# Kernel optimization log

Measured on AMD Instinct MI355X. Metric: run time of the kernel, lower is better.

## Reference

```python
import jax, jax.numpy as jnp
import numpy as np

B, S = 8, 512          # batch, seq_len
D, F = 1024, 2048      # d_model, head hidden dim
H = 16                 # num_tasks (= num heads)
V = 3000               # selfies vocab
O = 1                  # head output size
INIT = 0.02


def setup_inputs() -> dict:
    key = jax.random.key(0)
    ks = jax.random.split(key, 12)
    return {
        "selfies": jax.random.randint(ks[0], (B, S), 0, V),
        "tasks": jax.random.randint(ks[1], (B, S), 0, H + 1),  # 0 -> invalid (-1)
        "values": jax.random.normal(ks[2], (B, S), jnp.float32),
        "property_mask": jax.random.randint(ks[3], (B, S), 0, 2).astype(bool),
        # shared_base params (embed + FFN -> [B,S,D])
        "emb_selfies": jax.random.normal(ks[4], (V, D), jnp.float32) * INIT,
        "emb_tasks": jax.random.normal(ks[5], (H + 1, D), jnp.float32) * INIT,
        "val_vec": jax.random.normal(ks[6], (D,), jnp.float32) * INIT,
        "Ws": jax.random.normal(ks[7], (D, D), jnp.float32) * INIT,
        "bs": jnp.zeros((D,), jnp.float32),
        # stacked per-head MLP params: Linear(D,F) -> GELU -> Linear(F,O)
        "W1": jax.random.normal(ks[8], (H, D, F), jnp.float32) * INIT,
        "b1": jnp.zeros((H, F), jnp.float32),
        "W2": jax.random.normal(ks[9], (H, F, O), jnp.float32) * INIT,
        "b2": jnp.zeros((H, O), jnp.float32),
    }


def reference(selfies, tasks, values, property_mask,
              emb_selfies, emb_tasks, val_vec, Ws, bs, W1, b1, W2, b2):
    # ---- shared_base: embed + masked token features + FFN -> [B,S,D] ----
    h = (emb_selfies[selfies] + emb_tasks[tasks] + values[..., None] * val_vec)
    h = h * property_mask[..., None].astype(h.dtype)
    shared = jax.nn.gelu(h @ Ws + bs)                      # [B,S,D]

    # ---- routing: task token -> head index, 0 means invalid (-1) ----
    head_idx = jnp.where(tasks > 0, (tasks - 1) % H, -1)   # [B,S]

    # ---- each active head runs its MLP over the FULL shared_output ----
    hid = jax.nn.gelu(jnp.einsum('bsd,hdf->bshf', shared, W1) + b1)  # [B,S,H,F]
    heads_out = jnp.einsum('bshf,hfo->bsho', hid, W2) + b2           # [B,S,H,O]

    # ---- scatter/select per token by head index; invalid -> zeros ----
    idx = jnp.clip(head_idx, 0)
    out = jnp.take_along_axis(heads_out, idx[..., None, None], axis=2)[:, :, 0, :]
    return jnp.where(head_idx[..., None] >= 0, out, jnp.zeros_like(out))
```

## Files before the change

kernel.cpp:

```cpp
#include <hip/hip_runtime.h>
#include <hip/hip_bf16.h>

#define TOK 4096
#define DD  1024
#define FF  2048
#define NH  16

typedef short bf16x8 __attribute__((ext_vector_type(8)));
typedef float f32x4  __attribute__((ext_vector_type(4)));

__device__ __forceinline__ float gelu_f(float x) {
  float u = 0.7978845608028654f * (x + 0.044715f * x * x * x);
  float e = __expf(2.0f * u);
  return 0.5f * x * (2.0f - 2.0f / (e + 1.0f));
}

__device__ __forceinline__ unsigned short f2bf(float f) {
  union { float f; unsigned u; } v; v.f = f;
  unsigned r = v.u + 0x7FFF + ((v.u >> 16) & 1);
  return (unsigned short)(r >> 16);
}
__device__ __forceinline__ unsigned pack2(float a, float b) {
  return (unsigned)f2bf(a) | ((unsigned)f2bf(b) << 16);
}

__device__ __forceinline__ void load_lds16(const void* g, void* l) {
  __builtin_amdgcn_global_load_lds(
      (const __attribute__((address_space(1))) void*)g,
      (__attribute__((address_space(3))) void*)l, 16, 0, 0);
}

__global__ __launch_bounds__(256) void route_kernel(
    const int* __restrict__ tasks, const float* __restrict__ b2,
    int* __restrict__ counts, int* __restrict__ lists, float* __restrict__ out) {
  int t = blockIdx.x * 256 + threadIdx.x;
  if (t >= TOK) return;
  int task = tasks[t];
  if (task > 0) {
    int h = (task - 1) & (NH - 1);
    int pos = atomicAdd(&counts[h], 1);
    lists[h * TOK + pos] = t;
    out[t] = b2[h];
  } else {
    out[t] = 0.0f;
  }
}

__global__ __launch_bounds__(256) void prep_x(
    const int* __restrict__ selfies, const int* __restrict__ tasks,
    const float* __restrict__ values, const int* __restrict__ pmask,
    const float* __restrict__ emb_s, const float* __restrict__ emb_t,
    const float* __restrict__ val_vec, unsigned short* __restrict__ Xb) {
  int gid = blockIdx.x * 256 + threadIdx.x;
  int kc = (gid & 127) * 8;
  int t  = gid >> 7;
  int sid = selfies[t], tsk = tasks[t];
  float v = values[t];
  float msk = pmask[t] ? 1.0f : 0.0f;
  const float* ps = emb_s + (size_t)sid * DD + kc;
  const float* pt = emb_t + (size_t)tsk * DD + kc;
  const float* pv = val_vec + kc;
  float r[8];
#pragma unroll
  for (int j = 0; j < 8; j += 4) {
    float4 a = *(const float4*)(ps + j);
    float4 b = *(const float4*)(pt + j);
    float4 c = *(const float4*)(pv + j);
    r[j + 0] = (a.x + b.x + v * c.x) * msk;
    r[j + 1] = (a.y + b.y + v * c.y) * msk;
    r[j + 2] = (a.z + b.z + v * c.z) * msk;
    r[j + 3] = (a.w + b.w + v * c.w) * msk;
  }
  uint4 o;
  o.x = pack2(r[0], r[1]); o.y = pack2(r[2], r[3]);
  o.z = pack2(r[4], r[5]); o.w = pack2(r[6], r[7]);
  *(uint4*)(Xb + (size_t)gid * 8) = o;
}

__global__ __launch_bounds__(256) void prep_w(
    const float* __restrict__ Ws, const float* __restrict__ W1,
    unsigned short* __restrict__ Wsp, unsigned short* __restrict__ W1p) {
  int cid = blockIdx.x * 256 + threadIdx.x;
  const float* src;
  unsigned short* dst;
  int stride;
  if (cid < 16 * 128 * 32 * 64) {
    int lane = cid & 63, kc2 = (cid >> 6) & 31, nt = (cid >> 11) & 127, h = cid >> 18;
    src = W1 + ((size_t)h * DD + kc2 * 32 + (lane >> 4) * 8) * FF + nt * 16 + (lane & 15);
    dst = W1p + (size_t)cid * 8;
    stride = FF;
  } else {
    int cid2 = cid - 16 * 128 * 32 * 64;
    int lane = cid2 & 63, kc2 = (cid2 >> 6) & 31, nt = cid2 >> 11;
    src = Ws + ((size_t)kc2 * 32 + (lane >> 4) * 8) * DD + nt * 16 + (lane & 15);
    dst = Wsp + (size_t)cid2 * 8;
    stride = DD;
  }
  float r[8];
#pragma unroll
  for (int j = 0; j < 8; ++j) r[j] = src[(size_t)j * stride];
  uint4 o;
  o.x = pack2(r[0], r[1]); o.y = pack2(r[2], r[3]);
  o.z = pack2(r[4], r[5]); o.w = pack2(r[6], r[7]);
  *(uint4*)dst = o;
}

__global__ __launch_bounds__(256) void gemm1_mfma(
    const unsigned short* __restrict__ Xb, const unsigned short* __restrict__ Wsp,
    const float* __restrict__ bs, unsigned short* __restrict__ shared_bf) {
  __shared__ __align__(16) unsigned short As[2 * 4 * 64 * 8];
  __shared__ __align__(16) unsigned short Bs[2 * 8 * 64 * 8];

  const int tid = threadIdx.x;
  const int lane = tid & 63, w = tid >> 6;
  const int m0 = blockIdx.x * 64;
  const int n0 = blockIdx.y * 128;
  const int q = lane >> 4, c = lane & 15;

  const unsigned short* aSrc = Xb + (size_t)(m0 + w * 16 + c) * DD + q * 8;
  unsigned short* aDst0 = As + (size_t)(0 * 256 + w * 64 + lane) * 8;
  unsigned short* aDst1 = As + (size_t)(1 * 256 + w * 64 + lane) * 8;

  const unsigned short* bBase = Wsp + ((size_t)(blockIdx.y * 8 + w * 2)) * 32 * 512 + lane * 8;
  f32x4 acc[4][2] = {};

  for (int k0 = 0; k0 < DD; k0 += 64) {
    load_lds16(aSrc + k0, aDst0);
    load_lds16(aSrc + k0 + 32, aDst1);
    const unsigned short* bk = bBase + k0 * 16;
#pragma unroll
    for (int i = 0; i < 4; ++i) {
      int kk = i >> 1, t = i & 1;
      load_lds16(bk + (size_t)t * 16384 + kk * 512,
                 Bs + (size_t)(kk * 8 + w * 2 + t) * 512 + lane * 8);
    }
    __syncthreads();
#pragma unroll
    for (int kk = 0; kk < 2; ++kk) {
      bf16x8 a[4], b[2];
#pragma unroll
      for (int mt = 0; mt < 4; ++mt)
        a[mt] = *(const bf16x8*)(As + (size_t)((kk * 4 + mt) * 64 + lane) * 8);
#pragma unroll
      for (int t = 0; t < 2; ++t)
        b[t] = *(const bf16x8*)(Bs + (size_t)((kk * 8 + w * 2 + t) * 64 + lane) * 8);
#pragma unroll
      for (int mt = 0; mt < 4; ++mt)
#pragma unroll
        for (int t = 0; t < 2; ++t)
          acc[mt][t] = __builtin_amdgcn_mfma_f32_16x16x32_bf16(a[mt], b[t], acc[mt][t], 0, 0, 0);
    }
    __syncthreads();
  }

  float bsv[2];
#pragma unroll
  for (int t = 0; t < 2; ++t) bsv[t] = bs[n0 + w * 32 + t * 16 + c];
#pragma unroll
  for (int mt = 0; mt < 4; ++mt)
#pragma unroll
    for (int t = 0; t < 2; ++t)
#pragma unroll
      for (int r = 0; r < 4; ++r) {
        int row = m0 + mt * 16 + q * 4 + r;
        int col = n0 + w * 32 + t * 16 + c;
        shared_bf[(size_t)row * DD + col] = f2bf(gelu_f(acc[mt][t][r] + bsv[t]));
      }
}

__global__ __launch_bounds__(256) void gemm2_mfma(
    const unsigned short* __restrict__ shared_bf, const unsigned short* __restrict__ W1p,
    const float* __restrict__ b1, const float* __restrict__ W2,
    const int* __restrict__ counts, const int* __restrict__ lists,
    float* __restrict__ out) {
  const int h = blockIdx.z;
  const int nt_h = counts[h];
  const int m0 = blockIdx.x * 64;
  if (m0 >= nt_h) return;
  const int fc = blockIdx.y;

  __shared__ __align__(16) unsigned short As[2 * 4 * 64 * 8];
  __shared__ __align__(16) unsigned short Bs[2 * 16 * 64 * 8];
  __shared__ int   stok[64];
  __shared__ float red[4][68];

  const int tid = threadIdx.x;
  const int lane = tid & 63, w = tid >> 6;
  const int q = lane >> 4, c = lane & 15;

  if (tid < 64) {
    int i = m0 + tid;
    stok[tid] = (i < nt_h) ? lists[h * TOK + i] : -1;
  }
  __syncthreads();

  int tokr = stok[w * 16 + c];
  if (tokr < 0) tokr = 0;
  const unsigned short* aSrc = shared_bf + (size_t)tokr * DD + q * 8;
  unsigned short* aDst0 = As + (size_t)(0 * 256 + w * 64 + lane) * 8;
  unsigned short* aDst1 = As + (size_t)(1 * 256 + w * 64 + lane) * 8;

  const unsigned short* bBase =
      W1p + ((size_t)h * 128 + fc * 16 + w * 4) * 32 * 512 + lane * 8;

  f32x4 acc[4][4] = {};

  for (int k0 = 0; k0 < DD; k0 += 64) {
    load_lds16(aSrc + k0, aDst0);
    load_lds16(aSrc + k0 + 32, aDst1);
    const unsigned short* bk = bBase + k0 * 16;
#pragma unroll
    for (int i = 0; i < 8; ++i) {
      int kk = i >> 2, t = i & 3;
      load_lds16(bk + (size_t)t * 16384 + kk * 512,
                 Bs + (size_t)(kk * 16 + w * 4 + t) * 512 + lane * 8);
    }
    __syncthreads();
#pragma unroll
    for (int kk = 0; kk < 2; ++kk) {
      bf16x8 a[4], b[4];
#pragma unroll
      for (int mt = 0; mt < 4; ++mt)
        a[mt] = *(const bf16x8*)(As + (size_t)((kk * 4 + mt) * 64 + lane) * 8);
#pragma unroll
      for (int t = 0; t < 4; ++t)
        b[t] = *(const bf16x8*)(Bs + (size_t)((kk * 16 + w * 4 + t) * 64 + lane) * 8);
#pragma unroll
      for (int mt = 0; mt < 4; ++mt)
#pragma unroll
        for (int t = 0; t < 4; ++t)
          acc[mt][t] = __builtin_amdgcn_mfma_f32_16x16x32_bf16(a[mt], b[t], acc[mt][t], 0, 0, 0);
    }
    __syncthreads();
  }

  const float* b1h = b1 + (size_t)h * FF + fc * 256 + w * 64;
  const float* w2h = W2 + (size_t)h * FF + fc * 256 + w * 64;
  float b1v[4], w2v[4];
#pragma unroll
  for (int t = 0; t < 4; ++t) { b1v[t] = b1h[t * 16 + c]; w2v[t] = w2h[t * 16 + c]; }

#pragma unroll
  for (int mt = 0; mt < 4; ++mt)
#pragma unroll
    for (int r = 0; r < 4; ++r) {
      float s = 0.0f;
#pragma unroll
      for (int t = 0; t < 4; ++t)
        s += gelu_f(acc[mt][t][r] + b1v[t]) * w2v[t];
      s += __shfl_xor(s, 1);
      s += __shfl_xor(s, 2);
      s += __shfl_xor(s, 4);
      s += __shfl_xor(s, 8);
      if (c == 0) red[w][mt * 16 + q * 4 + r] = s;
    }
  __syncthreads();

  if (tid < 64) {
    int t = stok[tid];
    if (t >= 0) {
      float s = red[0][tid] + red[1][tid] + red[2][tid] + red[3][tid];
      atomicAdd(&out[t], s);
    }
  }
}

extern "C" void kernel_launch(void* const* d_in, const int* in_sizes, int n_in,
                              void* d_out, int out_size, void* d_ws, size_t ws_size,
                              hipStream_t stream) {
  const int*   selfies = (const int*)d_in[0];
  const int*   tasks   = (const int*)d_in[1];
  const float* values  = (const float*)d_in[2];
  const int*   pmask   = (const int*)d_in[3];
  const float* emb_s   = (const float*)d_in[4];
  const float* emb_t   = (const float*)d_in[5];
  const float* val_vec = (const float*)d_in[6];
  const float* Ws      = (const float*)d_in[7];
  const float* bs      = (const float*)d_in[8];
  const float* W1      = (const float*)d_in[9];
  const float* b1      = (const float*)d_in[10];
  const float* W2      = (const float*)d_in[11];
  const float* b2      = (const float*)d_in[12];
  float* out = (float*)d_out;

  char* ws = (char*)d_ws;
  unsigned short* Xb        = (unsigned short*)ws;
  unsigned short* shared_bf = (unsigned short*)(ws + (8u << 20));
  unsigned short* Wsp       = (unsigned short*)(ws + (16u << 20));
  unsigned short* W1p       = (unsigned short*)(ws + (18u << 20));
  int* counts = (int*)(ws + (82u << 20));
  int* lists  = (int*)(ws + (82u << 20) + 256);

  hipMemsetAsync(counts, 0, NH * sizeof(int), stream);
  route_kernel<<<TOK / 256, 256, 0, stream>>>(tasks, b2, counts, lists, out);
  prep_x<<<TOK * 128 / 256, 256, 0, stream>>>(selfies, tasks, values, pmask,
                                              emb_s, emb_t, val_vec, Xb);
  prep_w<<<(16 * 128 * 32 * 64 + 64 * 32 * 64) / 256, 256, 0, stream>>>(Ws, W1, Wsp, W1p);
  gemm1_mfma<<<dim3(TOK / 64, DD / 128), 256, 0, stream>>>(Xb, Wsp, bs, shared_bf);
  gemm2_mfma<<<dim3(8, FF / 256, NH), 256, 0, stream>>>(shared_bf, W1p, b1, W2,
                                                        counts, lists, out);
}
```

Before: 354.1 us.

## Stream B fragments via registers, double-buffer A in LDS, fuse routing into prep

Both GEMM kernels now load the pre-swizzled weight fragments straight from global memory into registers with one-stage prefetch, and keep only the activation tile in a double-buffered LDS array. This cuts LDS traffic and allows one barrier per k-step instead of two. The routing kernel is folded into the embedding prep kernel to save a launch. prep_w now has each thread convert two adjacent 16-column tiles, and launch bounds ask for 2 blocks per CU. The risks are higher register pressure from the bc/bn fragment arrays and uncoalesced-latency stalls on the direct global B loads.

```diff
diff --git a/kernel.cpp b/kernel.cpp
--- a/kernel.cpp
+++ b/kernel.cpp
@@ -30,31 +30,27 @@
       (__attribute__((address_space(3))) void*)l, 16, 0, 0);
 }
 
-__global__ __launch_bounds__(256) void route_kernel(
-    const int* __restrict__ tasks, const float* __restrict__ b2,
-    int* __restrict__ counts, int* __restrict__ lists, float* __restrict__ out) {
-  int t = blockIdx.x * 256 + threadIdx.x;
-  if (t >= TOK) return;
-  int task = tasks[t];
-  if (task > 0) {
-    int h = (task - 1) & (NH - 1);
-    int pos = atomicAdd(&counts[h], 1);
-    lists[h * TOK + pos] = t;
-    out[t] = b2[h];
-  } else {
-    out[t] = 0.0f;
-  }
-}
-
-__global__ __launch_bounds__(256) void prep_x(
+__global__ __launch_bounds__(256) void prep_xr(
     const int* __restrict__ selfies, const int* __restrict__ tasks,
     const float* __restrict__ values, const int* __restrict__ pmask,
     const float* __restrict__ emb_s, const float* __restrict__ emb_t,
-    const float* __restrict__ val_vec, unsigned short* __restrict__ Xb) {
+    const float* __restrict__ val_vec, const float* __restrict__ b2,
+    unsigned short* __restrict__ Xb, int* __restrict__ counts,
+    int* __restrict__ lists, float* __restrict__ out) {
   int gid = blockIdx.x * 256 + threadIdx.x;
   int kc = (gid & 127) * 8;
   int t  = gid >> 7;
   int sid = selfies[t], tsk = tasks[t];
+  if ((gid & 127) == 0) {
+    if (tsk > 0) {
+      int h = (tsk - 1) & (NH - 1);
+      int pos = atomicAdd(&counts[h], 1);
+      lists[h * TOK + pos] = t;
+      out[t] = b2[h];
+    } else {
+      out[t] = 0.0f;
+    }
+  }
   float v = values[t];
   float msk = pmask[t] ? 1.0f : 0.0f;
   const float* ps = emb_s + (size_t)sid * DD + kc;
@@ -80,36 +76,48 @@
 __global__ __launch_bounds__(256) void prep_w(
     const float* __restrict__ Ws, const float* __restrict__ W1,
     unsigned short* __restrict__ Wsp, unsigned short* __restrict__ W1p) {
-  int cid = blockIdx.x * 256 + threadIdx.x;
-  const float* src;
-  unsigned short* dst;
+  const int W1_PAIRS = 16 * 64 * 32 * 64;
+  int cid2 = blockIdx.x * 256 + threadIdx.x;
+  const float* src0;
+  unsigned short *dst0, *dst1;
   int stride;
-  if (cid < 16 * 128 * 32 * 64) {
-    int lane = cid & 63, kc2 = (cid >> 6) & 31, nt = (cid >> 11) & 127, h = cid >> 18;
-    src = W1 + ((size_t)h * DD + kc2 * 32 + (lane >> 4) * 8) * FF + nt * 16 + (lane & 15);
-    dst = W1p + (size_t)cid * 8;
+  if (cid2 < W1_PAIRS) {
+    int lane = cid2 & 63, kc2 = (cid2 >> 6) & 31, ntp = (cid2 >> 11) & 63, h = cid2 >> 17;
+    int q = lane >> 4, c = lane & 15;
+    src0 = W1 + ((size_t)h * DD + kc2 * 32 + q * 8) * FF + ntp * 32 + c;
+    size_t c0 = (((size_t)h * 128 + ntp * 2) * 32 + kc2) * 64 + lane;
+    dst0 = W1p + c0 * 8;
+    dst1 = W1p + (c0 + 32 * 64) * 8;
     stride = FF;
   } else {
-    int cid2 = cid - 16 * 128 * 32 * 64;
-    int lane = cid2 & 63, kc2 = (cid2 >> 6) & 31, nt = cid2 >> 11;
-    src = Ws + ((size_t)kc2 * 32 + (lane >> 4) * 8) * DD + nt * 16 + (lane & 15);
-    dst = Wsp + (size_t)cid2 * 8;
+    int cid3 = cid2 - W1_PAIRS;
+    int lane = cid3 & 63, kc2 = (cid3 >> 6) & 31, ntp = cid3 >> 11;
+    int q = lane >> 4, c = lane & 15;
+    src0 = Ws + ((size_t)kc2 * 32 + q * 8) * DD + ntp * 32 + c;
+    size_t c0 = ((size_t)(ntp * 2) * 32 + kc2) * 64 + lane;
+    dst0 = Wsp + c0 * 8;
+    dst1 = Wsp + (c0 + 32 * 64) * 8;
     stride = DD;
   }
-  float r[8];
-#pragma unroll
-  for (int j = 0; j < 8; ++j) r[j] = src[(size_t)j * stride];
-  uint4 o;
-  o.x = pack2(r[0], r[1]); o.y = pack2(r[2], r[3]);
-  o.z = pack2(r[4], r[5]); o.w = pack2(r[6], r[7]);
-  *(uint4*)dst = o;
-}
-
-__global__ __launch_bounds__(256) void gemm1_mfma(
+  float r0[8], r1[8];
+#pragma unroll
+  for (int j = 0; j < 8; ++j) {
+    r0[j] = src0[(size_t)j * stride];
+    r1[j] = src0[(size_t)j * stride + 16];
+  }
+  uint4 o0, o1;
+  o0.x = pack2(r0[0], r0[1]); o0.y = pack2(r0[2], r0[3]);
+  o0.z = pack2(r0[4], r0[5]); o0.w = pack2(r0[6], r0[7]);
+  o1.x = pack2(r1[0], r1[1]); o1.y = pack2(r1[2], r1[3]);
+  o1.z = pack2(r1[4], r1[5]); o1.w = pack2(r1[6], r1[7]);
+  *(uint4*)dst0 = o0;
+  *(uint4*)dst1 = o1;
+}
+
+__global__ __launch_bounds__(256, 2) void gemm1_mfma(
     const unsigned short* __restrict__ Xb, const unsigned short* __restrict__ Wsp,
     const float* __restrict__ bs, unsigned short* __restrict__ shared_bf) {
-  __shared__ __align__(16) unsigned short As[2 * 4 * 64 * 8];
-  __shared__ __align__(16) unsigned short Bs[2 * 8 * 64 * 8];
+  __shared__ __align__(16) unsigned short As[2][4096];
 
   const int tid = threadIdx.x;
   const int lane = tid & 63, w = tid >> 6;
@@ -118,39 +126,58 @@
   const int q = lane >> 4, c = lane & 15;
 
   const unsigned short* aSrc = Xb + (size_t)(m0 + w * 16 + c) * DD + q * 8;
-  unsigned short* aDst0 = As + (size_t)(0 * 256 + w * 64 + lane) * 8;
-  unsigned short* aDst1 = As + (size_t)(1 * 256 + w * 64 + lane) * 8;
-
-  const unsigned short* bBase = Wsp + ((size_t)(blockIdx.y * 8 + w * 2)) * 32 * 512 + lane * 8;
+
+  const unsigned short* bPtr[2];
+#pragma unroll
+  for (int t = 0; t < 2; ++t)
+    bPtr[t] = Wsp + (((size_t)(blockIdx.y * 8 + w * 2 + t) * 32) * 64 + lane) * 8;
+
   f32x4 acc[4][2] = {};
-
-  for (int k0 = 0; k0 < DD; k0 += 64) {
-    load_lds16(aSrc + k0, aDst0);
-    load_lds16(aSrc + k0 + 32, aDst1);
-    const unsigned short* bk = bBase + k0 * 16;
-#pragma unroll
-    for (int i = 0; i < 4; ++i) {
-      int kk = i >> 1, t = i & 1;
-      load_lds16(bk + (size_t)t * 16384 + kk * 512,
-                 Bs + (size_t)(kk * 8 + w * 2 + t) * 512 + lane * 8);
-    }
+  bf16x8 bc[2][2], bn[2][2];
+
+  load_lds16(aSrc, &As[0][(size_t)(0 * 256 + w * 64 + lane) * 8]);
+  load_lds16(aSrc + 32, &As[0][(size_t)(1 * 256 + w * 64 + lane) * 8]);
+#pragma unroll
+  for (int kk = 0; kk < 2; ++kk)
+#pragma unroll
+    for (int t = 0; t < 2; ++t)
+      bc[kk][t] = *(const bf16x8*)(bPtr[t] + (size_t)kk * 512);
+  __syncthreads();
+
+#pragma unroll
+  for (int s = 0; s < 16; ++s) {
+    const int p = s & 1;
+    bf16x8 a[2][4];
+#pragma unroll
+    for (int kk = 0; kk < 2; ++kk)
+#pragma unroll
+      for (int mt = 0; mt < 4; ++mt)
+        a[kk][mt] = *(const bf16x8*)&As[p][(size_t)((kk * 4 + mt) * 64 + lane) * 8];
+    if (s < 15) {
+      const int k1 = (s + 1) * 64;
+      load_lds16(aSrc + k1, &As[1 - p][(size_t)(0 * 256 + w * 64 + lane) * 8]);
+      load_lds16(aSrc + k1 + 32, &As[1 - p][(size_t)(1 * 256 + w * 64 + lane) * 8]);
+#pragma unroll
+      for (int kk = 0; kk < 2; ++kk)
+#pragma unroll
+        for (int t = 0; t < 2; ++t)
+          bn[kk][t] = *(const bf16x8*)(bPtr[t] + (size_t)((s + 1) * 2 + kk) * 512);
+    }
+#pragma unroll
+    for (int kk = 0; kk < 2; ++kk)
+#pragma unroll
+      for (int mt = 0; mt < 4; ++mt)
+#pragma unroll
+        for (int t = 0; t < 2; ++t)
+          acc[mt][t] = __builtin_amdgcn_mfma_f32_16x16x32_bf16(a[kk][mt], bc[kk][t], acc[mt][t], 0, 0, 0);
     __syncthreads();
-#pragma unroll
-    for (int kk = 0; kk < 2; ++kk) {
-      bf16x8 a[4], b[2];
-#pragma unroll
-      for (int mt = 0; mt < 4; ++mt)
-        a[mt] = *(const bf16x8*)(As + (size_t)((kk * 4 + mt) * 64 + lane) * 8);
-#pragma unroll
-      for (int t = 0; t < 2; ++t)
-        b[t] = *(const bf16x8*)(Bs + (size_t)((kk * 8 + w * 2 + t) * 64 + lane) * 8);
-#pragma unroll
-      for (int mt = 0; mt < 4; ++mt)
+    if (s < 15) {
+#pragma unroll
+      for (int kk = 0; kk < 2; ++kk)
 #pragma unroll
         for (int t = 0; t < 2; ++t)
-          acc[mt][t] = __builtin_amdgcn_mfma_f32_16x16x32_bf16(a[mt], b[t], acc[mt][t], 0, 0, 0);
-    }
-    __syncthreads();
+          bc[kk][t] = bn[kk][t];
+    }
   }
 
   float bsv[2];
@@ -168,7 +195,7 @@
       }
 }
 
-__global__ __launch_bounds__(256) void gemm2_mfma(
+__global__ __launch_bounds__(256, 2) void gemm2_mfma(
     const unsigned short* __restrict__ shared_bf, const unsigned short* __restrict__ W1p,
     const float* __restrict__ b1, const float* __restrict__ W2,
     const int* __restrict__ counts, const int* __restrict__ lists,
@@ -179,8 +206,7 @@
   if (m0 >= nt_h) return;
   const int fc = blockIdx.y;
 
-  __shared__ __align__(16) unsigned short As[2 * 4 * 64 * 8];
-  __shared__ __align__(16) unsigned short Bs[2 * 16 * 64 * 8];
+  __shared__ __align__(16) unsigned short As[2][4096];
   __shared__ int   stok[64];
   __shared__ float red[4][68];
 
@@ -197,41 +223,58 @@
   int tokr = stok[w * 16 + c];
   if (tokr < 0) tokr = 0;
   const unsigned short* aSrc = shared_bf + (size_t)tokr * DD + q * 8;
-  unsigned short* aDst0 = As + (size_t)(0 * 256 + w * 64 + lane) * 8;
-  unsigned short* aDst1 = As + (size_t)(1 * 256 + w * 64 + lane) * 8;
-
-  const unsigned short* bBase =
-      W1p + ((size_t)h * 128 + fc * 16 + w * 4) * 32 * 512 + lane * 8;
+
+  const unsigned short* bPtr[4];
+#pragma unroll
+  for (int t = 0; t < 4; ++t)
+    bPtr[t] = W1p + (((size_t)(h * 128 + fc * 16 + w * 4 + t) * 32) * 64 + lane) * 8;
 
   f32x4 acc[4][4] = {};
-
-  for (int k0 = 0; k0 < DD; k0 += 64) {
-    load_lds16(aSrc + k0, aDst0);
-    load_lds16(aSrc + k0 + 32, aDst1);
-    const unsigned short* bk = bBase + k0 * 16;
-#pragma unroll
-    for (int i = 0; i < 8; ++i) {
-      int kk = i >> 2, t = i & 3;
-      load_lds16(bk + (size_t)t * 16384 + kk * 512,
-                 Bs + (size_t)(kk * 16 + w * 4 + t) * 512 + lane * 8);
-    }
+  bf16x8 bc[2][4], bn[2][4];
+
+  load_lds16(aSrc, &As[0][(size_t)(0 * 256 + w * 64 + lane) * 8]);
+  load_lds16(aSrc + 32, &As[0][(size_t)(1 * 256 + w * 64 + lane) * 8]);
+#pragma unroll
+  for (int kk = 0; kk < 2; ++kk)
+#pragma unroll
+    for (int t = 0; t < 4; ++t)
+      bc[kk][t] = *(const bf16x8*)(bPtr[t] + (size_t)kk * 512);
+  __syncthreads();
+
+#pragma unroll
+  for (int s = 0; s < 16; ++s) {
+    const int p = s & 1;
+    bf16x8 a[2][4];
+#pragma unroll
+    for (int kk = 0; kk < 2; ++kk)
+#pragma unroll
+      for (int mt = 0; mt < 4; ++mt)
+        a[kk][mt] = *(const bf16x8*)&As[p][(size_t)((kk * 4 + mt) * 64 + lane) * 8];
+    if (s < 15) {
+      const int k1 = (s + 1) * 64;
+      load_lds16(aSrc + k1, &As[1 - p][(size_t)(0 * 256 + w * 64 + lane) * 8]);
+      load_lds16(aSrc + k1 + 32, &As[1 - p][(size_t)(1 * 256 + w * 64 + lane) * 8]);
+#pragma unroll
+      for (int kk = 0; kk < 2; ++kk)
+#pragma unroll
+        for (int t = 0; t < 4; ++t)
+          bn[kk][t] = *(const bf16x8*)(bPtr[t] + (size_t)((s + 1) * 2 + kk) * 512);
+    }
+#pragma unroll
+    for (int kk = 0; kk < 2; ++kk)
+#pragma unroll
+      for (int mt = 0; mt < 4; ++mt)
+#pragma unroll
+        for (int t = 0; t < 4; ++t)
+          acc[mt][t] = __builtin_amdgcn_mfma_f32_16x16x32_bf16(a[kk][mt], bc[kk][t], acc[mt][t], 0, 0, 0);
     __syncthreads();
-#pragma unroll
-    for (int kk = 0; kk < 2; ++kk) {
-      bf16x8 a[4], b[4];
-#pragma unroll
-      for (int mt = 0; mt < 4; ++mt)
-        a[mt] = *(const bf16x8*)(As + (size_t)((kk * 4 + mt) * 64 + lane) * 8);
-#pragma unroll
-      for (int t = 0; t < 4; ++t)
-        b[t] = *(const bf16x8*)(Bs + (size_t)((kk * 16 + w * 4 + t) * 64 + lane) * 8);
-#pragma unroll
-      for (int mt = 0; mt < 4; ++mt)
+    if (s < 15) {
+#pragma unroll
+      for (int kk = 0; kk < 2; ++kk)
 #pragma unroll
         for (int t = 0; t < 4; ++t)
-          acc[mt][t] = __builtin_amdgcn_mfma_f32_16x16x32_bf16(a[mt], b[t], acc[mt][t], 0, 0, 0);
-    }
-    __syncthreads();
+          bc[kk][t] = bn[kk][t];
+    }
   }
 
   const float* b1h = b1 + (size_t)h * FF + fc * 256 + w * 64;
@@ -292,10 +335,10 @@
   int* lists  = (int*)(ws + (82u << 20) + 256);
 
   hipMemsetAsync(counts, 0, NH * sizeof(int), stream);
-  route_kernel<<<TOK / 256, 256, 0, stream>>>(tasks, b2, counts, lists, out);
-  prep_x<<<TOK * 128 / 256, 256, 0, stream>>>(selfies, tasks, values, pmask,
-                                              emb_s, emb_t, val_vec, Xb);
-  prep_w<<<(16 * 128 * 32 * 64 + 64 * 32 * 64) / 256, 256, 0, stream>>>(Ws, W1, Wsp, W1p);
+  prep_xr<<<TOK * 128 / 256, 256, 0, stream>>>(selfies, tasks, values, pmask,
+                                               emb_s, emb_t, val_vec, b2,
+                                               Xb, counts, lists, out);
+  prep_w<<<(16 * 64 * 32 * 64 + 32 * 32 * 64) / 256, 256, 0, stream>>>(Ws, W1, Wsp, W1p);
   gemm1_mfma<<<dim3(TOK / 64, DD / 128), 256, 0, stream>>>(Xb, Wsp, bs, shared_bf);
   gemm2_mfma<<<dim3(8, FF / 256, NH), 256, 0, stream>>>(shared_bf, W1p, b1, W2,
                                                         counts, lists, out);
```

After: 388.3 us. 1.1x slower.
